# Kernel tuning notes

Measured on AMD Instinct MI355X. Metric: run time of the kernel, lower is better.

Reference implementation:

```python
import jax, jax.numpy as jnp
import numpy as np

DIM = 1024
N_HEADS = 16
HEAD_DIM = DIM // N_HEADS


def setup_inputs() -> dict:
    key = jax.random.key(0)
    ks = jax.random.split(key, 6)
    s = DIM ** -0.5
    return {
        "x": jax.random.normal(ks[0], (2, 2048, DIM), dtype=jnp.float32),
        "Wq": jax.random.normal(ks[1], (DIM, DIM), dtype=jnp.float32) * s,
        "Wk": jax.random.normal(ks[2], (DIM, DIM), dtype=jnp.float32) * s,
        "Wv": jax.random.normal(ks[3], (DIM, DIM), dtype=jnp.float32) * s,
        "Wo": jax.random.normal(ks[4], (DIM, DIM), dtype=jnp.float32) * s,
        "bo": jax.random.normal(ks[5], (DIM,), dtype=jnp.float32) * 0.01,
    }


def reference(x, Wq, Wk, Wv, Wo, bo):
    B, T, C = x.shape
    H, D = N_HEADS, HEAD_DIM
    # Linear(dim, dim, bias=False): y = x @ W^T
    q = (x @ Wq.T).reshape(B, T, H, D).transpose(0, 2, 1, 3)  # B H T D
    k = (x @ Wk.T).reshape(B, T, H, D).transpose(0, 2, 1, 3)
    v = (x @ Wv.T).reshape(B, T, H, D).transpose(0, 2, 1, 3)
    q = q * (D ** -0.5)
    attn = jnp.einsum('bhqd,bhkd->bhqk', q, k)  # B H T T
    causal_mask = jnp.triu(jnp.ones((T, T), dtype=bool), k=1)
    attn = jnp.where(causal_mask, -jnp.inf, attn)
    attn = jax.nn.softmax(attn, axis=-1)
    out = jnp.einsum('bhqk,bhkd->bhqd', attn, v)  # B H T D
    out = out.transpose(0, 2, 1, 3).reshape(B, T, C)
    return out @ Wo.T + bo
```

## Files before the change

### kernel.cpp

```cpp
#include <hip/hip_runtime.h>
#include <math.h>

typedef __attribute__((ext_vector_type(8))) short bf16x8;
typedef __attribute__((ext_vector_type(4))) float f32x4;

__device__ __forceinline__ ushort f2bf(float f) {
  union { float f; unsigned u; } v; v.f = f;
  return (ushort)((v.u + 0x8000u) >> 16);
}

__device__ __forceinline__ void g2l16(const void* g, void* l) {
  __builtin_amdgcn_global_load_lds((const __attribute__((address_space(1))) unsigned*)g,
                                   (__attribute__((address_space(3))) unsigned*)l, 16, 0, 0);
}

__global__ __launch_bounds__(256) void cast_all(const float* __restrict__ x,
                                                const float* __restrict__ Wq,
                                                const float* __restrict__ Wk,
                                                const float* __restrict__ Wv,
                                                const float* __restrict__ Wo,
                                                ushort* __restrict__ xbf,
                                                ushort* __restrict__ wcat,
                                                float4* __restrict__ O32) {
  int i = blockIdx.x * 256 + threadIdx.x;
  if (i < 1048576) {
    float4 v = ((const float4*)x)[i];
    ushort4 u; u.x = f2bf(v.x); u.y = f2bf(v.y); u.z = f2bf(v.z); u.w = f2bf(v.w);
    ((ushort4*)xbf)[i] = u;
  } else if (i < 2097152) {
    int j = i - 1048576;
    int sel = j >> 18;
    const float* src = (sel == 0) ? Wq : (sel == 1) ? Wk : (sel == 2) ? Wv : Wo;
    float scale = (sel == 0) ? 0.125f * 1.44269504088896f : 1.0f;
    float4 v = ((const float4*)src)[j & 0x3FFFF];
    ushort4 u;
    u.x = f2bf(v.x * scale); u.y = f2bf(v.y * scale);
    u.z = f2bf(v.z * scale); u.w = f2bf(v.w * scale);
    ((ushort4*)wcat)[j] = u;
  } else {
    O32[i - 2097152] = float4{0.f, 0.f, 0.f, 0.f};
  }
}

__global__ __launch_bounds__(256) void gemm_qkv(const ushort* __restrict__ A,
                                                const ushort* __restrict__ B,
                                                ushort* __restrict__ C3) {
  const int K = 1024;
  __shared__ __align__(16) ushort As[2][128 * 32];
  __shared__ __align__(16) ushort Bs[2][128 * 32];
  const int m0 = blockIdx.y * 128, n0 = blockIdx.x * 128;
  const int tid = threadIdx.x, lane = tid & 63, wid = tid >> 6;
  const int quad = lane >> 4, lc = lane & 15;
  const int lrow = lane >> 2, lcol = (lane & 3) * 8;
  const int wm = (wid >> 1) * 64, wn = (wid & 1) * 64;

  f32x4 acc[4][4] = {};

  auto stage = [&](int k0, int nb) {
    const ushort* Ag = A + (size_t)(m0 + wid * 32 + lrow) * K + k0 + lcol;
    g2l16(Ag, &As[nb][wid * 1024]);
    g2l16(Ag + (size_t)16 * K, &As[nb][wid * 1024 + 512]);
    const ushort* Bg = B + (size_t)(n0 + wid * 32 + lrow) * K + k0 + lcol;
    g2l16(Bg, &Bs[nb][wid * 1024]);
    g2l16(Bg + (size_t)16 * K, &Bs[nb][wid * 1024 + 512]);
  };

  stage(0, 0);
  for (int k0 = 0; k0 < K; k0 += 32) {
    const int nb = (k0 >> 5) & 1;
    __syncthreads();
    if (k0 + 32 < K) stage(k0 + 32, nb ^ 1);

    bf16x8 af[4], bfr[4];
#pragma unroll
    for (int t = 0; t < 4; t++)
      af[t] = *(const bf16x8*)&As[nb][(wm + t * 16 + lc) * 32 + quad * 8];
#pragma unroll
    for (int t = 0; t < 4; t++)
      bfr[t] = *(const bf16x8*)&Bs[nb][(wn + t * 16 + lc) * 32 + quad * 8];
#pragma unroll
    for (int mt = 0; mt < 4; mt++)
#pragma unroll
      for (int nt = 0; nt < 4; nt++)
        acc[mt][nt] = __builtin_amdgcn_mfma_f32_16x16x32_bf16(af[mt], bfr[nt], acc[mt][nt], 0, 0, 0);
  }

#pragma unroll
  for (int mt = 0; mt < 4; mt++) {
#pragma unroll
    for (int r = 0; r < 4; r++) {
      int row = m0 + wm + mt * 16 + quad * 4 + r;
#pragma unroll
      for (int nt = 0; nt < 4; nt++) {
        int col = n0 + wn + nt * 16 + lc;
        size_t dst = ((size_t)(col >> 10) << 22) + (size_t)row * 1024 + (col & 1023);
        C3[dst] = f2bf(acc[mt][nt][r]);
      }
    }
  }
}

__global__ __launch_bounds__(256) void gemm_proj(const ushort* __restrict__ A,
                                                 const ushort* __restrict__ B,
                                                 float* __restrict__ C,
                                                 const float* __restrict__ bias) {
  const int K = 1024;
  __shared__ __align__(16) ushort As[2][2][128 * 32];
  __shared__ __align__(16) ushort Bs[2][2][64 * 32];
  const int m0 = blockIdx.y * 128, n0 = blockIdx.x * 64;
  const int tid = threadIdx.x, lane = tid & 63, wid = tid >> 6;
  const int quad = lane >> 4, lc = lane & 15;
  const int lrow = lane >> 2, lcol = (lane & 3) * 8;
  const int wm = (wid >> 1) * 64, wn = (wid & 1) * 32;

  f32x4 acc[4][2] = {};

  auto stage = [&](int k0, int nb) {
    const ushort* Ag = A + (size_t)(m0 + wid * 32 + lrow) * K + k0 + lcol;
    g2l16(Ag,                       &As[nb][0][wid * 1024]);
    g2l16(Ag + (size_t)16 * K,      &As[nb][0][wid * 1024 + 512]);
    g2l16(Ag + 32,                  &As[nb][1][wid * 1024]);
    g2l16(Ag + (size_t)16 * K + 32, &As[nb][1][wid * 1024 + 512]);
    const ushort* Bg = B + (size_t)(n0 + wid * 16 + lrow) * K + k0 + lcol;
    g2l16(Bg,      &Bs[nb][0][wid * 512]);
    g2l16(Bg + 32, &Bs[nb][1][wid * 512]);
  };

  stage(0, 0);
  for (int k0 = 0; k0 < K; k0 += 64) {
    const int nb = (k0 >> 6) & 1;
    __syncthreads();
    if (k0 + 64 < K) stage(k0 + 64, nb ^ 1);

#pragma unroll
    for (int ks = 0; ks < 2; ks++) {
      bf16x8 af[4], bfr[2];
#pragma unroll
      for (int t = 0; t < 4; t++)
        af[t] = *(const bf16x8*)&As[nb][ks][(wm + t * 16 + lc) * 32 + quad * 8];
#pragma unroll
      for (int t = 0; t < 2; t++)
        bfr[t] = *(const bf16x8*)&Bs[nb][ks][(wn + t * 16 + lc) * 32 + quad * 8];
#pragma unroll
      for (int mt = 0; mt < 4; mt++)
#pragma unroll
        for (int nt = 0; nt < 2; nt++)
          acc[mt][nt] = __builtin_amdgcn_mfma_f32_16x16x32_bf16(af[mt], bfr[nt], acc[mt][nt], 0, 0, 0);
    }
  }

#pragma unroll
  for (int mt = 0; mt < 4; mt++) {
#pragma unroll
    for (int r = 0; r < 4; r++) {
      int row = m0 + wm + mt * 16 + quad * 4 + r;
#pragma unroll
      for (int nt = 0; nt < 2; nt++) {
        int col = n0 + wn + nt * 16 + lc;
        C[(size_t)row * 1024 + col] = acc[mt][nt][r] + bias[col];
      }
    }
  }
}

__global__ __launch_bounds__(256) void transpose_v(const ushort* __restrict__ Vb,
                                                   ushort* __restrict__ Vt,
                                                   float4* __restrict__ L32z) {
  __shared__ ushort tile[64][72];
  const int bh = blockIdx.y, b = bh >> 4, h = bh & 15;
  const int tt = blockIdx.x;
  const int tid = threadIdx.x;
  if (bh == 0) {
    int base = (tt * 256 + tid) * 2;
    L32z[base]     = float4{0.f, 0.f, 0.f, 0.f};
    L32z[base + 1] = float4{0.f, 0.f, 0.f, 0.f};
  }
#pragma unroll
  for (int i = 0; i < 2; i++) {
    int idx = i * 256 + tid;
    int trow = idx >> 3;
    int dcol = (idx & 7) * 8;
    uint4 v = *(const uint4*)(Vb + (size_t)(b * 2048 + tt * 64 + trow) * 1024 + h * 64 + dcol);
    ushort e[8]; *(uint4*)e = v;
#pragma unroll
    for (int j = 0; j < 8; j++) tile[dcol + j][trow] = e[j];
  }
  __syncthreads();
#pragma unroll
  for (int i = 0; i < 2; i++) {
    int idx = i * 256 + tid;
    int drow = idx >> 3;
    int tloc = (idx & 7) * 8;
    uint4 v = *(const uint4*)&tile[drow][tloc];
    *(uint4*)(Vt + (size_t)bh * 131072 + (size_t)drow * 2048 + tt * 64 + tloc) = v;
  }
}

__global__ __launch_bounds__(128, 3) void attn_kernel(const ushort* __restrict__ Qb,
                                                      const ushort* __restrict__ Kb,
                                                      const ushort* __restrict__ Vt,
                                                      float* __restrict__ O32,
                                                      float* __restrict__ L32) {
  __shared__ __align__(16) ushort Ks[2][64 * 32];
  __shared__ __align__(16) ushort Vs[2][64 * 32];
  __shared__ __align__(16) ushort Ps[2][32][72];

  const int bh = blockIdx.y, b = bh >> 4, h = bh & 15;
  const int f = 79 - (int)blockIdx.x;
  int qi, ci;
  if (f < 8)       { qi = f;                 ci = 0; }
  else if (f < 24) { int g = f - 8;  qi = 8  + (g >> 1); ci = g & 1; }
  else if (f < 48) { int g = f - 24; int q3 = g / 3; qi = 16 + q3; ci = g - 3 * q3; }
  else             { int g = f - 48; qi = 24 + (g >> 2); ci = g & 3; }
  const int t0 = ci * 8;
  const int t1 = min(t0 + 8, qi + 1);

  const int tid = threadIdx.x, lane = tid & 63, wid = tid >> 6;
  const int quad = lane >> 4, lc = lane & 15;
  const int lrow = lane >> 2, lcol = (lane & 3) * 8;
  const int qbw = qi * 64 + wid * 32;

  const size_t kbase = (size_t)(b * 2048) * 1024 + h * 64;
  const size_t vbase = (size_t)bh * 131072;

  bf16x8 qf[2][2];
#pragma unroll
  for (int t = 0; t < 2; t++) {
    const ushort* Qp = Qb + kbase + (size_t)(qbw + t * 16 + lc) * 1024;
    qf[t][0] = *(const bf16x8*)(Qp + quad * 8);
    qf[t][1] = *(const bf16x8*)(Qp + 32 + quad * 8);
  }

  bf16x8 ones;
#pragma unroll
  for (int j = 0; j < 8; j++) ones[j] = (short)0x3f80;

  f32x4 o_acc[2][4] = {};
  f32x4 l_acc[2] = {};

  for (int kt = t0; kt < t1; kt++) {
    const int kb = kt * 64;
    __syncthreads();
#pragma unroll
    for (int j = 0; j < 4; j++) {
      const ushort* gK = Kb + kbase + (size_t)(kb + j * 16 + lrow) * 1024 + wid * 32 + lcol;
      g2l16(gK, &Ks[wid][j * 512]);
      const ushort* gV = Vt + vbase + (size_t)(j * 16 + lrow) * 2048 + kb + wid * 32 + lcol;
      g2l16(gV, &Vs[wid][j * 512]);
    }
    __syncthreads();

    bf16x8 kf[4][2];
#pragma unroll
    for (int c = 0; c < 4; c++) {
      kf[c][0] = *(const bf16x8*)&Ks[0][(c * 16 + lc) * 32 + quad * 8];
      kf[c][1] = *(const bf16x8*)&Ks[1][(c * 16 + lc) * 32 + quad * 8];
    }

#pragma unroll
    for (int c = 0; c < 4; c++) {
#pragma unroll
      for (int t = 0; t < 2; t++) {
        f32x4 z = {};
        z = __builtin_amdgcn_mfma_f32_16x16x32_bf16(qf[t][0], kf[c][0], z, 0, 0, 0);
        z = __builtin_amdgcn_mfma_f32_16x16x32_bf16(qf[t][1], kf[c][1], z, 0, 0, 0);
        const bool diag = (kb + 63 > qbw + t * 16);
#pragma unroll
        for (int r = 0; r < 4; r++) {
          float sv = z[r];
          if (diag && (kb + c * 16 + lc > qbw + t * 16 + quad * 4 + r)) sv = -1e30f;
          Ps[wid][t * 16 + quad * 4 + r][c * 16 + lc] = f2bf(__builtin_amdgcn_exp2f(sv));
        }
      }
    }
    __asm__ volatile("s_waitcnt lgkmcnt(0)" ::: "memory");
    bf16x8 ap[2][2];
#pragma unroll
    for (int t = 0; t < 2; t++) {
      ap[t][0] = *(const bf16x8*)&Ps[wid][t * 16 + lc][quad * 8];
      ap[t][1] = *(const bf16x8*)&Ps[wid][t * 16 + lc][32 + quad * 8];
    }

#pragma unroll
    for (int t = 0; t < 2; t++) {
      l_acc[t] = __builtin_amdgcn_mfma_f32_16x16x32_bf16(ap[t][0], ones, l_acc[t], 0, 0, 0);
      l_acc[t] = __builtin_amdgcn_mfma_f32_16x16x32_bf16(ap[t][1], ones, l_acc[t], 0, 0, 0);
    }

#pragma unroll
    for (int nt = 0; nt < 4; nt++) {
      bf16x8 vb0 = *(const bf16x8*)&Vs[0][(nt * 16 + lc) * 32 + quad * 8];
      bf16x8 vb1 = *(const bf16x8*)&Vs[1][(nt * 16 + lc) * 32 + quad * 8];
#pragma unroll
      for (int t = 0; t < 2; t++) {
        o_acc[t][nt] = __builtin_amdgcn_mfma_f32_16x16x32_bf16(ap[t][0], vb0, o_acc[t][nt], 0, 0, 0);
        o_acc[t][nt] = __builtin_amdgcn_mfma_f32_16x16x32_bf16(ap[t][1], vb1, o_acc[t][nt], 0, 0, 0);
      }
    }
  }

#pragma unroll
  for (int t = 0; t < 2; t++) {
    if (lc == 0) {
#pragma unroll
      for (int r = 0; r < 4; r++)
        atomicAdd(&L32[(size_t)bh * 2048 + qbw + t * 16 + quad * 4 + r], l_acc[t][r]);
    }
#pragma unroll
    for (int r = 0; r < 4; r++) {
      size_t orow = ((size_t)(b * 2048) + qbw + t * 16 + quad * 4 + r) * 1024 + h * 64 + lc;
#pragma unroll
      for (int nt = 0; nt < 4; nt++)
        atomicAdd(&O32[orow + nt * 16], o_acc[t][nt][r]);
    }
  }
}

__global__ __launch_bounds__(256) void normalize_kernel(const float* __restrict__ O32,
                                                        const float* __restrict__ L32,
                                                        ushort* __restrict__ Out) {
  const int row = blockIdx.x;
  const int tid = threadIdx.x;
  const int col = tid * 4;
  const int b = row >> 11, t = row & 2047, h = col >> 6;
  const float inv = 1.0f / L32[(size_t)(b * 16 + h) * 2048 + t];
  float4 o = ((const float4*)(O32 + (size_t)row * 1024))[tid];
  ushort4 u;
  u.x = f2bf(o.x * inv); u.y = f2bf(o.y * inv);
  u.z = f2bf(o.z * inv); u.w = f2bf(o.w * inv);
  ((ushort4*)(Out + (size_t)row * 1024))[tid] = u;
}

extern "C" void kernel_launch(void* const* d_in, const int* in_sizes, int n_in,
                              void* d_out, int out_size, void* d_ws, size_t ws_size,
                              hipStream_t stream) {
  const float* x  = (const float*)d_in[0];
  const float* Wq = (const float*)d_in[1];
  const float* Wk = (const float*)d_in[2];
  const float* Wv = (const float*)d_in[3];
  const float* Wo = (const float*)d_in[4];
  const float* bo = (const float*)d_in[5];
  float* out = (float*)d_out;

  char* ws = (char*)d_ws;
  ushort* xbf  = (ushort*)(ws);
  ushort* wcat = (ushort*)(ws + (8ull  << 20));
  ushort* qkv  = (ushort*)(ws + (16ull << 20));
  ushort* Qp   = qkv;
  ushort* Kp   = qkv + (1ull << 22);
  ushort* Vp   = qkv + (2ull << 22);
  ushort* Vt   = (ushort*)(ws);
  float*  L32  = (float*)(ws + (12ull << 20));
  float*  O32  = out;
  ushort* attn_out = Qp;

  cast_all<<<12288, 256, 0, stream>>>(x, Wq, Wk, Wv, Wo, xbf, wcat, (float4*)O32);

  gemm_qkv<<<dim3(24, 32), 256, 0, stream>>>(xbf, wcat, qkv);

  transpose_v<<<dim3(32, 32), 256, 0, stream>>>(Vp, Vt, (float4*)L32);

  attn_kernel<<<dim3(80, 32), 128, 0, stream>>>(Qp, Kp, Vt, O32, L32);

  normalize_kernel<<<4096, 256, 0, stream>>>(O32, L32, attn_out);

  gemm_proj<<<dim3(16, 32), 256, 0, stream>>>(
      attn_out, wcat + (size_t)3072 * 1024, out, bo);
}
```

Before: 206.2 us.

## Fuse V transpose into QKV GEMM epilogue and double-buffer attention K/V tiles

The QKV GEMM epilogue now writes V blocks transposed through shared memory straight into the Vt layout. This removes the separate transpose kernel and its extra read and write of V. L32 zeroing moves to a hipMemsetAsync. The attention kernel double-buffers its K/V LDS tiles so the next tile's global-to-LDS loads overlap with compute, at the cost of doubling K/V shared memory, which may reduce occupancy.

```diff
diff --git a/kernel.cpp b/kernel.cpp
--- a/kernel.cpp
+++ b/kernel.cpp
@@ -44,10 +44,12 @@
 
 __global__ __launch_bounds__(256) void gemm_qkv(const ushort* __restrict__ A,
                                                 const ushort* __restrict__ B,
-                                                ushort* __restrict__ C3) {
+                                                ushort* __restrict__ C3,
+                                                ushort* __restrict__ Vt) {
   const int K = 1024;
-  __shared__ __align__(16) ushort As[2][128 * 32];
-  __shared__ __align__(16) ushort Bs[2][128 * 32];
+  __shared__ __align__(16) ushort smem[17408];
+  ushort* As = smem;
+  ushort* Bs = smem + 8192;
   const int m0 = blockIdx.y * 128, n0 = blockIdx.x * 128;
   const int tid = threadIdx.x, lane = tid & 63, wid = tid >> 6;
   const int quad = lane >> 4, lc = lane & 15;
@@ -58,11 +60,11 @@
 
   auto stage = [&](int k0, int nb) {
     const ushort* Ag = A + (size_t)(m0 + wid * 32 + lrow) * K + k0 + lcol;
-    g2l16(Ag, &As[nb][wid * 1024]);
-    g2l16(Ag + (size_t)16 * K, &As[nb][wid * 1024 + 512]);
+    g2l16(Ag, &As[nb * 4096 + wid * 1024]);
+    g2l16(Ag + (size_t)16 * K, &As[nb * 4096 + wid * 1024 + 512]);
     const ushort* Bg = B + (size_t)(n0 + wid * 32 + lrow) * K + k0 + lcol;
-    g2l16(Bg, &Bs[nb][wid * 1024]);
-    g2l16(Bg + (size_t)16 * K, &Bs[nb][wid * 1024 + 512]);
+    g2l16(Bg, &Bs[nb * 4096 + wid * 1024]);
+    g2l16(Bg + (size_t)16 * K, &Bs[nb * 4096 + wid * 1024 + 512]);
   };
 
   stage(0, 0);
@@ -74,10 +76,10 @@
     bf16x8 af[4], bfr[4];
 #pragma unroll
     for (int t = 0; t < 4; t++)
-      af[t] = *(const bf16x8*)&As[nb][(wm + t * 16 + lc) * 32 + quad * 8];
+      af[t] = *(const bf16x8*)&As[nb * 4096 + (wm + t * 16 + lc) * 32 + quad * 8];
 #pragma unroll
     for (int t = 0; t < 4; t++)
-      bfr[t] = *(const bf16x8*)&Bs[nb][(wn + t * 16 + lc) * 32 + quad * 8];
+      bfr[t] = *(const bf16x8*)&Bs[nb * 4096 + (wn + t * 16 + lc) * 32 + quad * 8];
 #pragma unroll
     for (int mt = 0; mt < 4; mt++)
 #pragma unroll
@@ -85,17 +87,42 @@
         acc[mt][nt] = __builtin_amdgcn_mfma_f32_16x16x32_bf16(af[mt], bfr[nt], acc[mt][nt], 0, 0, 0);
   }
 
-#pragma unroll
-  for (int mt = 0; mt < 4; mt++) {
-#pragma unroll
-    for (int r = 0; r < 4; r++) {
-      int row = m0 + wm + mt * 16 + quad * 4 + r;
-#pragma unroll
-      for (int nt = 0; nt < 4; nt++) {
-        int col = n0 + wn + nt * 16 + lc;
-        size_t dst = ((size_t)(col >> 10) << 22) + (size_t)row * 1024 + (col & 1023);
-        C3[dst] = f2bf(acc[mt][nt][r]);
-      }
+  const int sel = n0 >> 10;
+  if (sel < 2) {
+#pragma unroll
+    for (int mt = 0; mt < 4; mt++) {
+#pragma unroll
+      for (int r = 0; r < 4; r++) {
+        int row = m0 + wm + mt * 16 + quad * 4 + r;
+#pragma unroll
+        for (int nt = 0; nt < 4; nt++) {
+          int col = n0 + wn + nt * 16 + lc;
+          size_t dst = ((size_t)sel << 22) + (size_t)row * 1024 + (col & 1023);
+          C3[dst] = f2bf(acc[mt][nt][r]);
+        }
+      }
+    }
+  } else {
+    __syncthreads();
+#pragma unroll
+    for (int mt = 0; mt < 4; mt++)
+#pragma unroll
+      for (int r = 0; r < 4; r++) {
+        int tl = wm + mt * 16 + quad * 4 + r;
+#pragma unroll
+        for (int nt = 0; nt < 4; nt++)
+          smem[(wn + nt * 16 + lc) * 136 + tl] = f2bf(acc[mt][nt][r]);
+      }
+    __syncthreads();
+    const int hd0 = n0 - 2048, b = m0 >> 11, t_base = m0 & 2047;
+#pragma unroll
+    for (int i = 0; i < 8; i++) {
+      int idx = i * 256 + tid;
+      int dl = idx >> 4, tc = (idx & 15) * 8;
+      uint4 v = *(const uint4*)&smem[dl * 136 + tc];
+      int hd = hd0 + dl;
+      *(uint4*)(Vt + (size_t)(b * 16 + (hd >> 6)) * 131072 +
+                (size_t)(hd & 63) * 2048 + t_base + tc) = v;
     }
   }
 }
@@ -163,46 +190,13 @@
   }
 }
 
-__global__ __launch_bounds__(256) void transpose_v(const ushort* __restrict__ Vb,
-                                                   ushort* __restrict__ Vt,
-                                                   float4* __restrict__ L32z) {
-  __shared__ ushort tile[64][72];
-  const int bh = blockIdx.y, b = bh >> 4, h = bh & 15;
-  const int tt = blockIdx.x;
-  const int tid = threadIdx.x;
-  if (bh == 0) {
-    int base = (tt * 256 + tid) * 2;
-    L32z[base]     = float4{0.f, 0.f, 0.f, 0.f};
-    L32z[base + 1] = float4{0.f, 0.f, 0.f, 0.f};
-  }
-#pragma unroll
-  for (int i = 0; i < 2; i++) {
-    int idx = i * 256 + tid;
-    int trow = idx >> 3;
-    int dcol = (idx & 7) * 8;
-    uint4 v = *(const uint4*)(Vb + (size_t)(b * 2048 + tt * 64 + trow) * 1024 + h * 64 + dcol);
-    ushort e[8]; *(uint4*)e = v;
-#pragma unroll
-    for (int j = 0; j < 8; j++) tile[dcol + j][trow] = e[j];
-  }
-  __syncthreads();
-#pragma unroll
-  for (int i = 0; i < 2; i++) {
-    int idx = i * 256 + tid;
-    int drow = idx >> 3;
-    int tloc = (idx & 7) * 8;
-    uint4 v = *(const uint4*)&tile[drow][tloc];
-    *(uint4*)(Vt + (size_t)bh * 131072 + (size_t)drow * 2048 + tt * 64 + tloc) = v;
-  }
-}
-
 __global__ __launch_bounds__(128, 3) void attn_kernel(const ushort* __restrict__ Qb,
                                                       const ushort* __restrict__ Kb,
                                                       const ushort* __restrict__ Vt,
                                                       float* __restrict__ O32,
                                                       float* __restrict__ L32) {
-  __shared__ __align__(16) ushort Ks[2][64 * 32];
-  __shared__ __align__(16) ushort Vs[2][64 * 32];
+  __shared__ __align__(16) ushort Ks[2][2][2048];
+  __shared__ __align__(16) ushort Vs[2][2][2048];
   __shared__ __align__(16) ushort Ps[2][32][72];
 
   const int bh = blockIdx.y, b = bh >> 4, h = bh & 15;
@@ -238,23 +232,28 @@
   f32x4 o_acc[2][4] = {};
   f32x4 l_acc[2] = {};
 
+  auto stage = [&](int kb, int nb) {
+#pragma unroll
+    for (int j = 0; j < 4; j++) {
+      const ushort* gK = Kb + kbase + (size_t)(kb + j * 16 + lrow) * 1024 + wid * 32 + lcol;
+      g2l16(gK, &Ks[nb][wid][j * 512]);
+      const ushort* gV = Vt + vbase + (size_t)(j * 16 + lrow) * 2048 + kb + wid * 32 + lcol;
+      g2l16(gV, &Vs[nb][wid][j * 512]);
+    }
+  };
+
+  stage(t0 * 64, 0);
   for (int kt = t0; kt < t1; kt++) {
     const int kb = kt * 64;
-    __syncthreads();
-#pragma unroll
-    for (int j = 0; j < 4; j++) {
-      const ushort* gK = Kb + kbase + (size_t)(kb + j * 16 + lrow) * 1024 + wid * 32 + lcol;
-      g2l16(gK, &Ks[wid][j * 512]);
-      const ushort* gV = Vt + vbase + (size_t)(j * 16 + lrow) * 2048 + kb + wid * 32 + lcol;
-      g2l16(gV, &Vs[wid][j * 512]);
-    }
-    __syncthreads();
+    const int nb = (kt - t0) & 1;
+    __syncthreads();
+    if (kt + 1 < t1) stage(kb + 64, nb ^ 1);
 
     bf16x8 kf[4][2];
 #pragma unroll
     for (int c = 0; c < 4; c++) {
-      kf[c][0] = *(const bf16x8*)&Ks[0][(c * 16 + lc) * 32 + quad * 8];
-      kf[c][1] = *(const bf16x8*)&Ks[1][(c * 16 + lc) * 32 + quad * 8];
+      kf[c][0] = *(const bf16x8*)&Ks[nb][0][(c * 16 + lc) * 32 + quad * 8];
+      kf[c][1] = *(const bf16x8*)&Ks[nb][1][(c * 16 + lc) * 32 + quad * 8];
     }
 
 #pragma unroll
@@ -289,8 +288,8 @@
 
 #pragma unroll
     for (int nt = 0; nt < 4; nt++) {
-      bf16x8 vb0 = *(const bf16x8*)&Vs[0][(nt * 16 + lc) * 32 + quad * 8];
-      bf16x8 vb1 = *(const bf16x8*)&Vs[1][(nt * 16 + lc) * 32 + quad * 8];
+      bf16x8 vb0 = *(const bf16x8*)&Vs[nb][0][(nt * 16 + lc) * 32 + quad * 8];
+      bf16x8 vb1 = *(const bf16x8*)&Vs[nb][1][(nt * 16 + lc) * 32 + quad * 8];
 #pragma unroll
       for (int t = 0; t < 2; t++) {
         o_acc[t][nt] = __builtin_amdgcn_mfma_f32_16x16x32_bf16(ap[t][0], vb0, o_acc[t][nt], 0, 0, 0);
@@ -348,17 +347,16 @@
   ushort* qkv  = (ushort*)(ws + (16ull << 20));
   ushort* Qp   = qkv;
   ushort* Kp   = qkv + (1ull << 22);
-  ushort* Vp   = qkv + (2ull << 22);
-  ushort* Vt   = (ushort*)(ws);
-  float*  L32  = (float*)(ws + (12ull << 20));
+  ushort* Vt   = qkv + (2ull << 22);
+  float*  L32  = (float*)ws;
   float*  O32  = out;
   ushort* attn_out = Qp;
 
   cast_all<<<12288, 256, 0, stream>>>(x, Wq, Wk, Wv, Wo, xbf, wcat, (float4*)O32);
 
-  gemm_qkv<<<dim3(24, 32), 256, 0, stream>>>(xbf, wcat, qkv);
-
-  transpose_v<<<dim3(32, 32), 256, 0, stream>>>(Vp, Vt, (float4*)L32);
+  gemm_qkv<<<dim3(24, 32), 256, 0, stream>>>(xbf, wcat, qkv, Vt);
+
+  hipMemsetAsync(L32, 0, (size_t)32 * 2048 * 4, stream);
 
   attn_kernel<<<dim3(80, 32), 128, 0, stream>>>(Qp, Kp, Vt, O32, L32);
 
```

Measured after the change: 216.6 us. 5.1% more time.
